# Kernel optimization log

Measured on AMD Instinct MI355X. Metric: run time of the kernel, lower is better.

## Reference

```python
import jax, jax.numpy as jnp
import numpy as np

N_EDGES = 1_600_000
N_NODES = 100_000
IN_CH = 32
OUT_CH = 64
TOTAL_DIM = IN_CH * 4 * 3  # 4 aggregators x 3 scalers


def setup_inputs() -> dict:
    key = jax.random.key(0)
    k1, k2, k3, k4 = jax.random.split(key, 4)
    messages = jax.random.normal(k1, (N_EDGES, IN_CH), dtype=jnp.float32)
    dst = jax.random.randint(k2, (N_EDGES,), 0, N_NODES, dtype=jnp.int64)
    W = jax.random.normal(k3, (OUT_CH, TOTAL_DIM), dtype=jnp.float32) / np.sqrt(TOTAL_DIM)
    b = jax.random.normal(k4, (OUT_CH,), dtype=jnp.float32) * 0.01
    return {"messages": messages, "dst": dst, "num_nodes": N_NODES, "W": W, "b": b}


def reference(messages, dst, num_nodes, W, b):
    # degree (clamped to >=1, matching scatter_count)
    ones = jnp.ones(dst.shape[0], dtype=messages.dtype)
    deg_raw = jax.ops.segment_sum(ones, dst, num_segments=num_nodes)
    deg = jnp.maximum(deg_raw, 1.0)

    # mean
    s = jax.ops.segment_sum(messages, dst, num_segments=num_nodes)  # [N, d]
    mean = s / deg[:, None]

    # max / min with empty-segment -> 0 (torch fills -inf/+inf then zeroes)
    mx = jax.ops.segment_max(messages, dst, num_segments=num_nodes)
    mx = jnp.where(jnp.isneginf(mx), jnp.zeros_like(mx), mx)
    mn = jax.ops.segment_min(messages, dst, num_segments=num_nodes)
    mn = jnp.where(jnp.isposinf(mn), jnp.zeros_like(mn), mn)

    # std: mean of squared deviations from per-node mean
    sq_diff = (messages - mean[dst]) ** 2
    var = jax.ops.segment_sum(sq_diff, dst, num_segments=num_nodes) / deg[:, None]
    std = jnp.sqrt(var + 1e-8)

    amp = jnp.log(deg + 1.0)[:, None]       # amplification scaler
    att = (1.0 / (deg + 1.0))[:, None]      # attenuation scaler

    results = []
    for agg in (mean, mx, mn, std):  # order matches default aggregators
        results.extend([agg, agg * amp, agg * att])  # identity, amp, att
    combined = jnp.concatenate(results, axis=-1)  # [N, 12*d]
    return combined @ W.T + b
```

## Files before the change

### kernel.cpp

```cpp
#include <hip/hip_runtime.h>
#include <math.h>

#define NE 1600000
#define NN 100000
#define NBKT 391
#define BINCH 8192
#define NBINBLK ((NE + BINCH - 1) / BINCH)

typedef __attribute__((ext_vector_type(8))) short bf16x8;
typedef __attribute__((ext_vector_type(4))) float f32x4;

static __device__ inline short f2bf(float f) {
  unsigned u = __float_as_uint(f);
  u += 0x7FFFu + ((u >> 16) & 1u);
  return (short)(u >> 16);
}

__global__ void k_init0(int* __restrict__ bktcnt) {
  int t = threadIdx.x;
  if (t < NBKT) bktcnt[t] = 0;
}

__global__ __launch_bounds__(256) void k_bktcount(const int* __restrict__ dst,
                                                  int* __restrict__ bktcnt) {
  __shared__ int hist[NBKT];
  int t = threadIdx.x;
  for (int j = t; j < NBKT; j += 256) hist[j] = 0;
  __syncthreads();
  int start = blockIdx.x * BINCH;
  int lim = min(BINCH, NE - start);
  for (int j = t; j < lim; j += 256) atomicAdd(&hist[dst[start + j] >> 8], 1);
  __syncthreads();
  for (int j = t; j < NBKT; j += 256) {
    int h = hist[j];
    if (h) atomicAdd(&bktcnt[j], h);
  }
}

__global__ void k_bktscan(const int* __restrict__ bktcnt, int* __restrict__ bktoff,
                          int* __restrict__ bkcur, int* __restrict__ off) {
  __shared__ int s[512];
  int t = threadIdx.x;
  int v = (t < NBKT) ? bktcnt[t] : 0;
  s[t] = v;
  __syncthreads();
  for (int d = 1; d < 512; d <<= 1) {
    int x = (t >= d) ? s[t - d] : 0;
    __syncthreads();
    s[t] += x;
    __syncthreads();
  }
  if (t < NBKT) {
    int ex = s[t] - v;
    bktoff[t] = ex;
    bkcur[t] = ex;
  }
  if (t == 0) {
    bktoff[NBKT] = NE;
    off[NN] = NE;
  }
}

__global__ __launch_bounds__(256) void k_bin(const int* __restrict__ dst,
                                             int* __restrict__ bkcur,
                                             int2* __restrict__ pairs) {
  __shared__ int sdst[BINCH];
  __shared__ int hist[NBKT];
  int t = threadIdx.x;
  int start = blockIdx.x * BINCH;
  int lim = min(BINCH, NE - start);
  for (int j = t; j < NBKT; j += 256) hist[j] = 0;
  __syncthreads();
  for (int j = t; j < lim; j += 256) {
    int d = dst[start + j];
    sdst[j] = d;
    atomicAdd(&hist[d >> 8], 1);
  }
  __syncthreads();
  for (int j = t; j < NBKT; j += 256) {
    int h = hist[j];
    hist[j] = h ? atomicAdd(&bkcur[j], h) : 0;
  }
  __syncthreads();
  for (int j = t; j < lim; j += 256) {
    int d = sdst[j];
    int q = atomicAdd(&hist[d >> 8], 1);
    pairs[q] = make_int2(d, start + j);
  }
}

__global__ __launch_bounds__(256) void k_build(const int2* __restrict__ pairs,
                                               const int* __restrict__ bktoff,
                                               int* __restrict__ off,
                                               int* __restrict__ eid) {
  __shared__ int cnt[256];
  __shared__ int loc[256];
  int b = blockIdx.x, t = threadIdx.x;
  int base = bktoff[b];
  int m = bktoff[b + 1] - base;
  cnt[t] = 0;
  __syncthreads();
  for (int i = t; i < m; i += 256) atomicAdd(&cnt[pairs[base + i].x & 255], 1);
  __syncthreads();
  int v = cnt[t];
  loc[t] = v;
  __syncthreads();
  for (int d = 1; d < 256; d <<= 1) {
    int x = (t >= d) ? loc[t - d] : 0;
    __syncthreads();
    loc[t] += x;
    __syncthreads();
  }
  int ex = base + loc[t] - v;
  int node = b * 256 + t;
  if (node < NN) off[node] = ex;
  __syncthreads();
  loc[t] = ex;
  __syncthreads();
  for (int i = t; i < m; i += 256) {
    int2 pe = pairs[base + i];
    int p = atomicAdd(&loc[pe.x & 255], 1);
    eid[p] = pe.y;
  }
}

__global__ __launch_bounds__(512) void k_fused(const float* __restrict__ msg,
                                               const int* __restrict__ off,
                                               const int* __restrict__ eid,
                                               const float* __restrict__ W,
                                               const float* __restrict__ bias,
                                               float* __restrict__ out) {
  __shared__ short Bf[12 * 4 * 64 * 8];
  for (int j = threadIdx.x; j < 12 * 4 * 64 * 8; j += 512) {
    int i = j & 7, l = (j >> 3) & 63, ct = (j >> 9) & 3, kt = j >> 11;
    int col = ct * 16 + (l & 15);
    int k = kt * 32 + (l >> 4) * 8 + i;
    Bf[j] = f2bf(W[col * 384 + k]);
  }
  __syncthreads();

  int wid = threadIdx.x >> 6, lane = threadIdx.x & 63;
  int r = lane & 15, oct = lane >> 4;
  int nb = (blockIdx.x * 8 + wid) * 16;
  if (nb >= NN) return;
  int node = nb + r;

  int e0 = off[node], e1 = off[node + 1];

  float sv[8], qv[8], xv[8], nv[8];
#pragma unroll
  for (int i = 0; i < 8; i++) {
    sv[i] = 0.f;
    qv[i] = 0.f;
    xv[i] = -INFINITY;
    nv[i] = INFINITY;
  }

  int p = e0;
  int nfull = (e1 - e0) >> 2;
  for (int it = 0; it < nfull; ++it, p += 4) {
    int ea0 = eid[p], ea1 = eid[p + 1], ea2 = eid[p + 2], ea3 = eid[p + 3];
    const f32x4* r0 = (const f32x4*)(msg + (size_t)ea0 * 32 + oct * 8);
    const f32x4* r1 = (const f32x4*)(msg + (size_t)ea1 * 32 + oct * 8);
    const f32x4* r2 = (const f32x4*)(msg + (size_t)ea2 * 32 + oct * 8);
    const f32x4* r3 = (const f32x4*)(msg + (size_t)ea3 * 32 + oct * 8);
    f32x4 va0 = r0[0], vb0 = r0[1];
    f32x4 va1 = r1[0], vb1 = r1[1];
    f32x4 va2 = r2[0], vb2 = r2[1];
    f32x4 va3 = r3[0], vb3 = r3[1];
#pragma unroll
    for (int i = 0; i < 4; i++) {
      float w0 = va0[i], w1 = va1[i], w2 = va2[i], w3 = va3[i];
      sv[i] += w0 + w1 + w2 + w3;
      qv[i] += w0 * w0 + w1 * w1 + w2 * w2 + w3 * w3;
      xv[i] = fmaxf(fmaxf(xv[i], fmaxf(w0, w1)), fmaxf(w2, w3));
      nv[i] = fminf(fminf(nv[i], fminf(w0, w1)), fminf(w2, w3));
      float z0 = vb0[i], z1 = vb1[i], z2 = vb2[i], z3 = vb3[i];
      sv[i + 4] += z0 + z1 + z2 + z3;
      qv[i + 4] += z0 * z0 + z1 * z1 + z2 * z2 + z3 * z3;
      xv[i + 4] = fmaxf(fmaxf(xv[i + 4], fmaxf(z0, z1)), fmaxf(z2, z3));
      nv[i + 4] = fminf(fminf(nv[i + 4], fminf(z0, z1)), fminf(z2, z3));
    }
  }
  for (; p < e1; ++p) {
    int e = eid[p];
    const f32x4* rp = (const f32x4*)(msg + (size_t)e * 32 + oct * 8);
    f32x4 a = rp[0], b = rp[1];
#pragma unroll
    for (int i = 0; i < 4; i++) {
      float v0 = a[i], v1 = b[i];
      sv[i] += v0;
      qv[i] += v0 * v0;
      xv[i] = fmaxf(xv[i], v0);
      nv[i] = fminf(nv[i], v0);
      sv[i + 4] += v1;
      qv[i + 4] += v1 * v1;
      xv[i + 4] = fmaxf(xv[i + 4], v1);
      nv[i + 4] = fminf(nv[i + 4], v1);
    }
  }

  float degr = (float)(e1 - e0);
  float deg = fmaxf(degr, 1.f);
  float inv = 1.f / deg;
  float amp = logf(deg + 1.f);
  float att = 1.f / (deg + 1.f);

#pragma unroll
  for (int i = 0; i < 8; i++) {
    float me = sv[i] * inv;
    float va = fmaxf(qv[i] * inv - me * me, 0.f);
    sv[i] = me;
    qv[i] = sqrtf(va + 1e-8f);
    xv[i] = (xv[i] == -INFINITY) ? 0.f : xv[i];
    nv[i] = (nv[i] == INFINITY) ? 0.f : nv[i];
  }

  f32x4 acc[4] = {{0.f, 0.f, 0.f, 0.f},
                  {0.f, 0.f, 0.f, 0.f},
                  {0.f, 0.f, 0.f, 0.f},
                  {0.f, 0.f, 0.f, 0.f}};
  float scal[3] = {1.f, amp, att};
  const bf16x8* Bp = (const bf16x8*)Bf;
#pragma unroll
  for (int kt = 0; kt < 12; kt++) {
    const float* ag = (kt < 3) ? sv : (kt < 6) ? xv : (kt < 9) ? nv : qv;
    float sc = scal[kt % 3];
    bf16x8 af;
#pragma unroll
    for (int i = 0; i < 8; i++) af[i] = f2bf(ag[i] * sc);
#pragma unroll
    for (int ct = 0; ct < 4; ct++) {
      acc[ct] = __builtin_amdgcn_mfma_f32_16x16x32_bf16(af, Bp[(kt * 4 + ct) * 64 + lane],
                                                        acc[ct], 0, 0, 0);
    }
  }

#pragma unroll
  for (int ct = 0; ct < 4; ct++) {
    int ocol = ct * 16 + r;
    float bb = bias[ocol];
#pragma unroll
    for (int j = 0; j < 4; j++) {
      int orow = nb + oct * 4 + j;
      out[orow * 64 + ocol] = acc[ct][j] + bb;
    }
  }
}

extern "C" void kernel_launch(void* const* d_in, const int* in_sizes, int n_in,
                              void* d_out, int out_size, void* d_ws, size_t ws_size,
                              hipStream_t stream) {
  const float* msg = (const float*)d_in[0];
  const int* dst = (const int*)d_in[1];
  const float* W = (const float*)d_in[3];
  const float* bias = (const float*)d_in[4];
  float* out = (float*)d_out;

  int* wsi = (int*)d_ws;
  int2* pairs = (int2*)wsi;
  int* eid = wsi + 2 * NE;
  int* off = wsi + 3 * NE;
  int* bktcnt = wsi + 3 * NE + NN + 1;
  int* bktoff = bktcnt + NBKT;
  int* bkcur = bktoff + NBKT + 1;

  k_init0<<<1, 512, 0, stream>>>(bktcnt);
  k_bktcount<<<NBINBLK, 256, 0, stream>>>(dst, bktcnt);
  k_bktscan<<<1, 512, 0, stream>>>(bktcnt, bktoff, bkcur, off);
  k_bin<<<NBINBLK, 256, 0, stream>>>(dst, bkcur, pairs);
  k_build<<<NBKT, 256, 0, stream>>>(pairs, bktoff, off, eid);
  k_fused<<<(NN / 16 + 7) / 8, 512, 0, stream>>>(msg, off, eid, W, bias, out);
}
```

Baseline: 128.1 us.

## Precompute bf16 weight fragments once and read them from global in fused kernel

Moves the per-block W-to-bf16 fragment conversion into a separate one-time prep kernel, so the fused kernel reads prepacked fragments from global/L2 and needs no shared memory or block barrier. Blocks shrink to 256 threads with a minimum-occupancy hint, and the edge-id loads are software-prefetched one iteration ahead in the gather loop. This removes the redundant per-block conversion of 24K weights and the LDS occupancy limit, at the cost of an extra launch and global loads of B fragments during the MFMA phase.

```diff
diff --git a/kernel.cpp b/kernel.cpp
--- a/kernel.cpp
+++ b/kernel.cpp
@@ -19,6 +19,16 @@
 __global__ void k_init0(int* __restrict__ bktcnt) {
   int t = threadIdx.x;
   if (t < NBKT) bktcnt[t] = 0;
+}
+
+__global__ void k_wprep(const float* __restrict__ W, short* __restrict__ Wf) {
+  int j = blockIdx.x * 256 + threadIdx.x;
+  if (j < 12 * 4 * 64 * 8) {
+    int i = j & 7, l = (j >> 3) & 63, ct = (j >> 9) & 3, kt = j >> 11;
+    int col = ct * 16 + (l & 15);
+    int k = kt * 32 + (l >> 4) * 8 + i;
+    Wf[j] = f2bf(W[col * 384 + k]);
+  }
 }
 
 __global__ __launch_bounds__(256) void k_bktcount(const int* __restrict__ dst,
@@ -124,24 +134,15 @@
   }
 }
 
-__global__ __launch_bounds__(512) void k_fused(const float* __restrict__ msg,
-                                               const int* __restrict__ off,
-                                               const int* __restrict__ eid,
-                                               const float* __restrict__ W,
-                                               const float* __restrict__ bias,
-                                               float* __restrict__ out) {
-  __shared__ short Bf[12 * 4 * 64 * 8];
-  for (int j = threadIdx.x; j < 12 * 4 * 64 * 8; j += 512) {
-    int i = j & 7, l = (j >> 3) & 63, ct = (j >> 9) & 3, kt = j >> 11;
-    int col = ct * 16 + (l & 15);
-    int k = kt * 32 + (l >> 4) * 8 + i;
-    Bf[j] = f2bf(W[col * 384 + k]);
-  }
-  __syncthreads();
-
+__global__ __launch_bounds__(256, 6) void k_fused(const float* __restrict__ msg,
+                                                  const int* __restrict__ off,
+                                                  const int* __restrict__ eid,
+                                                  const short* __restrict__ Wf,
+                                                  const float* __restrict__ bias,
+                                                  float* __restrict__ out) {
   int wid = threadIdx.x >> 6, lane = threadIdx.x & 63;
   int r = lane & 15, oct = lane >> 4;
-  int nb = (blockIdx.x * 8 + wid) * 16;
+  int nb = (blockIdx.x * 4 + wid) * 16;
   if (nb >= NN) return;
   int node = nb + r;
 
@@ -156,14 +157,29 @@
     nv[i] = INFINITY;
   }
 
+  const float* mbase = msg + oct * 8;
   int p = e0;
   int nfull = (e1 - e0) >> 2;
-  for (int it = 0; it < nfull; ++it, p += 4) {
-    int ea0 = eid[p], ea1 = eid[p + 1], ea2 = eid[p + 2], ea3 = eid[p + 3];
-    const f32x4* r0 = (const f32x4*)(msg + (size_t)ea0 * 32 + oct * 8);
-    const f32x4* r1 = (const f32x4*)(msg + (size_t)ea1 * 32 + oct * 8);
-    const f32x4* r2 = (const f32x4*)(msg + (size_t)ea2 * 32 + oct * 8);
-    const f32x4* r3 = (const f32x4*)(msg + (size_t)ea3 * 32 + oct * 8);
+  int ea0 = 0, ea1 = 0, ea2 = 0, ea3 = 0;
+  if (nfull > 0) {
+    ea0 = eid[p];
+    ea1 = eid[p + 1];
+    ea2 = eid[p + 2];
+    ea3 = eid[p + 3];
+  }
+  for (int it = 0; it < nfull; ++it) {
+    int c0 = ea0, c1 = ea1, c2 = ea2, c3 = ea3;
+    p += 4;
+    if (it + 1 < nfull) {
+      ea0 = eid[p];
+      ea1 = eid[p + 1];
+      ea2 = eid[p + 2];
+      ea3 = eid[p + 3];
+    }
+    const f32x4* r0 = (const f32x4*)(mbase + (size_t)c0 * 32);
+    const f32x4* r1 = (const f32x4*)(mbase + (size_t)c1 * 32);
+    const f32x4* r2 = (const f32x4*)(mbase + (size_t)c2 * 32);
+    const f32x4* r3 = (const f32x4*)(mbase + (size_t)c3 * 32);
     f32x4 va0 = r0[0], vb0 = r0[1];
     f32x4 va1 = r1[0], vb1 = r1[1];
     f32x4 va2 = r2[0], vb2 = r2[1];
@@ -184,7 +200,7 @@
   }
   for (; p < e1; ++p) {
     int e = eid[p];
-    const f32x4* rp = (const f32x4*)(msg + (size_t)e * 32 + oct * 8);
+    const f32x4* rp = (const f32x4*)(mbase + (size_t)e * 32);
     f32x4 a = rp[0], b = rp[1];
 #pragma unroll
     for (int i = 0; i < 4; i++) {
@@ -221,19 +237,23 @@
                   {0.f, 0.f, 0.f, 0.f},
                   {0.f, 0.f, 0.f, 0.f}};
   float scal[3] = {1.f, amp, att};
-  const bf16x8* Bp = (const bf16x8*)Bf;
+  const bf16x8* Bp = (const bf16x8*)Wf;
 #pragma unroll
   for (int kt = 0; kt < 12; kt++) {
     const float* ag = (kt < 3) ? sv : (kt < 6) ? xv : (kt < 9) ? nv : qv;
     float sc = scal[kt % 3];
+    bf16x8 b0 = Bp[(kt * 4 + 0) * 64 + lane];
+    bf16x8 b1 = Bp[(kt * 4 + 1) * 64 + lane];
+    bf16x8 b2 = Bp[(kt * 4 + 2) * 64 + lane];
+    bf16x8 b3 = Bp[(kt * 4 + 3) * 64 + lane];
     bf16x8 af;
 #pragma unroll
     for (int i = 0; i < 8; i++) af[i] = f2bf(ag[i] * sc);
-#pragma unroll
-    for (int ct = 0; ct < 4; ct++) {
-      acc[ct] = __builtin_amdgcn_mfma_f32_16x16x32_bf16(af, Bp[(kt * 4 + ct) * 64 + lane],
-                                                        acc[ct], 0, 0, 0);
-    }
+    acc[0] = __builtin_amdgcn_mfma_f32_16x16x32_bf16(af, b0, acc[0], 0, 0, 0);
+    acc[1] = __builtin_amdgcn_mfma_f32_16x16x32_bf16(af, b1, acc[1], 0, 0, 0);
+    acc[2] = __builtin_amdgcn_mfma_f32_16x16x32_bf16(af, b2, acc[2], 0, 0, 0);
+    acc[3] = __builtin_amdgcn_mfma_f32_16x16x32_bf16(af, b3, acc[3], 0, 0, 0);
+    __builtin_amdgcn_sched_barrier(0);
   }
 
 #pragma unroll
@@ -264,11 +284,13 @@
   int* bktcnt = wsi + 3 * NE + NN + 1;
   int* bktoff = bktcnt + NBKT;
   int* bkcur = bktoff + NBKT + 1;
+  short* Wfrag = (short*)(bkcur + NBKT);
 
   k_init0<<<1, 512, 0, stream>>>(bktcnt);
+  k_wprep<<<96, 256, 0, stream>>>(W, Wfrag);
   k_bktcount<<<NBINBLK, 256, 0, stream>>>(dst, bktcnt);
   k_bktscan<<<1, 512, 0, stream>>>(bktcnt, bktoff, bkcur, off);
   k_bin<<<NBINBLK, 256, 0, stream>>>(dst, bkcur, pairs);
   k_build<<<NBKT, 256, 0, stream>>>(pairs, bktoff, off, eid);
-  k_fused<<<(NN / 16 + 7) / 8, 512, 0, stream>>>(msg, off, eid, W, bias, out);
-}
+  k_fused<<<(NN / 16 + 3) / 4, 256, 0, stream>>>(msg, off, eid, Wfrag, bias, out);
+}
```

Result: no change. 128.5 us (+0.3%).
